# Kernel tuning notes

Measured on AMD Instinct MI355X. Metric: run time of the kernel, lower is better.

The kernel has to match this reference:

```python
import jax, jax.numpy as jnp
import numpy as np

N = 100_000      # nodes
E = 3_200_000    # edges (avg degree 32)
F_IN = 128       # in_channels
HID = 64         # hidden_channels
G = 64           # graphs in batch


def setup_inputs() -> dict:
    key = jax.random.key(0)
    k0, k1, k2, k3 = jax.random.split(key, 4)
    x = jax.random.normal(k0, (N, F_IN), jnp.float32)
    edge_index = jax.random.randint(k1, (2, E), 0, N, dtype=jnp.int32)
    # sorted graph assignment, every graph non-empty
    batch = (jnp.arange(N, dtype=jnp.int32) * G) // N
    W1 = jax.random.normal(k2, (F_IN, HID), jnp.float32) * (1.0 / np.sqrt(F_IN))
    b1 = jnp.zeros((HID,), jnp.float32)
    W2 = jax.random.normal(k3, (HID, 1), jnp.float32) * (1.0 / np.sqrt(HID))
    b2 = jnp.zeros((1,), jnp.float32)
    return {"x": x, "edge_index": edge_index, "batch": batch,
            "W1": W1, "b1": b1, "W2": W2, "b2": b2}


def gcn_layer(x, src, dst, W, b):
    """GCNConv: add self-loops, symmetric deg^-1/2 norm, scatter-add, bias."""
    h = x @ W  # transform first (smaller messages)
    loops = jnp.arange(N, dtype=src.dtype)
    s = jnp.concatenate([src, loops])
    d = jnp.concatenate([dst, loops])
    deg = jax.ops.segment_sum(jnp.ones(s.shape[0], x.dtype), d, num_segments=N)
    dinv = jnp.where(deg > 0, jax.lax.rsqrt(deg), 0.0)
    norm = dinv[s] * dinv[d]                         # [E+N]
    out = jax.ops.segment_sum(h[s] * norm[:, None], d, num_segments=N)
    return out + b


def reference(x, edge_index, batch, W1, b1, W2, b2):
    src, dst = edge_index[0], edge_index[1]
    h = jax.nn.relu(gcn_layer(x, src, dst, W1, b1))
    h = gcn_layer(h, src, dst, W2, b2)               # [N, 1]
    counts = jax.ops.segment_sum(jnp.ones(N, jnp.int32), batch, num_segments=G)
    big_node_idx = jnp.cumsum(counts) - 1            # last node of each graph
    return h[big_node_idx].squeeze(-1)               # [G]
```

## Files before the change

kernel.cpp:

```cpp
#include <hip/hip_runtime.h>

#define N_NODES 100000
#define N_EDGES 3200000
#define F_IN    128
#define HID     64
#define NGRAPH  64

#define NBUK    196
#define BSHIFT  9
#define BCAP    18432
#define CHUNK   5120
#define NBLK_A  625
#define SLICES  8
#define NWORDS  3200
#define MAXDEG  96
#define NIDCAP  4096
#define L2CAP   8192
#define NBLK_X  2048


__device__ __forceinline__ bool is_big(int v, const int* __restrict__ batch) {
    return (v == N_NODES - 1) || (batch[v] != batch[v + 1]);
}
__device__ __forceinline__ float dinv_of(int degv) {
    return rsqrtf((float)(degv + 1));
}

__global__ void k_init(const int* __restrict__ batch, unsigned* __restrict__ bigmask,
                       unsigned* __restrict__ nmask, int* __restrict__ nid_of,
                       int* __restrict__ nlist, int* __restrict__ counters,
                       float* __restrict__ out) {
    if (blockIdx.x == 0 && threadIdx.x < NGRAPH) out[threadIdx.x] = 0.f;
    int v = blockIdx.x * 256 + threadIdx.x;
    if (v >= N_NODES) return;
    if (is_big(v, batch)) {
        atomicOr(&bigmask[v >> 5], 1u << (v & 31));
        atomicOr(&nmask[v >> 5], 1u << (v & 31));
        int p = atomicAdd(&counters[2], 1);
        nid_of[v] = p;
        nlist[p]  = v;
    }
}

__global__ __launch_bounds__(256) void k_partA(const int* __restrict__ src,
        const int* __restrict__ dst, const unsigned* __restrict__ bigmask,
        unsigned* __restrict__ nmask, unsigned* __restrict__ plist,
        int* __restrict__ bcnt, int2* __restrict__ l2list, int* __restrict__ counters) {
    __shared__ unsigned staged[CHUNK];
    __shared__ unsigned char sbkt[CHUNK];
    __shared__ int hist4[4][NBUK];
    __shared__ int startb[256];
    __shared__ int curb[NBUK], gbasea[NBUK];
    __shared__ int wsum[4];
    __shared__ int2 l2buf[64];
    __shared__ int l2n, l2base;
    const int t = threadIdx.x;
    const int lane = t & 63;
    const int w = t >> 6;
    for (int i = t; i < NBUK; i += 256) {
        hist4[0][i] = 0; hist4[1][i] = 0; hist4[2][i] = 0; hist4[3][i] = 0;
    }
    if (t == 0) l2n = 0;
    __syncthreads();

    const int E0 = blockIdx.x * CHUNK;
    const int4* s4 = (const int4*)(src + E0);
    const int4* d4 = (const int4*)(dst + E0);
    int vloc[20]; unsigned pk[20];
#pragma unroll
    for (int it = 0; it < 5; ++it) {
        int4 dd = d4[t + it * 256];
        int4 ss = s4[t + it * 256];
        int vv[4] = {dd.x, dd.y, dd.z, dd.w};
        int uu[4] = {ss.x, ss.y, ss.z, ss.w};
#pragma unroll
        for (int j = 0; j < 4; ++j) {
            int v = vv[j], u = uu[j];
            vloc[it * 4 + j] = v;
            pk[it * 4 + j] = ((unsigned)u << BSHIFT) | (unsigned)(v & 511);
            atomicAdd(&hist4[w][v >> BSHIFT], 1);
            if ((bigmask[v >> 5] >> (v & 31)) & 1) {
                atomicOr(&nmask[u >> 5], 1u << (u & 31));
                int p = atomicAdd(&l2n, 1);
                if (p < 64) l2buf[p] = make_int2(u, v);
            }
        }
    }
    __syncthreads();
    int c = 0;
    if (t < NBUK) c = hist4[0][t] + hist4[1][t] + hist4[2][t] + hist4[3][t];
    int sc = c;
#pragma unroll
    for (int off = 1; off < 64; off <<= 1) {
        int y = __shfl_up(sc, off, 64);
        if (lane >= off) sc += y;
    }
    if (lane == 63) wsum[w] = sc;
    __syncthreads();
    int pre = 0;
#pragma unroll
    for (int k = 0; k < 4; ++k) pre += (k < w) ? wsum[k] : 0;
    int excl = pre + sc - c;
    startb[t] = excl;
    if (t < NBUK) {
        curb[t]   = excl;
        gbasea[t] = atomicAdd(&bcnt[t], c);
    }
    if (t == 0 && l2n > 0) {
        int ln = l2n; if (ln > 64) ln = 64;
        l2base = atomicAdd(&counters[1], ln);
    }
    __syncthreads();
    {
        int ln = l2n; if (ln > 64) ln = 64;
        for (int i = t; i < ln; i += 256) {
            int p = l2base + i;
            if (p < L2CAP) l2list[p] = l2buf[i];
        }
    }
#pragma unroll
    for (int it = 0; it < 20; ++it) {
        int b = vloc[it] >> BSHIFT;
        int pos = atomicAdd(&curb[b], 1);
        staged[pos] = pk[it];
        sbkt[pos]   = (unsigned char)b;
    }
    __syncthreads();
    for (int i = t; i < CHUNK; i += 256) {
        int b = sbkt[i];
        int s = gbasea[b] + (i - startb[b]);
        if (s < BCAP) plist[(size_t)b * BCAP + s] = staged[i];
    }
}

__global__ void k_buildnid(const unsigned* __restrict__ nmask,
                           const unsigned* __restrict__ bigmask,
                           int* __restrict__ nid_of, int* __restrict__ nlist,
                           int* __restrict__ counters) {
    int w = blockIdx.x * 256 + threadIdx.x;
    unsigned m = (w < NWORDS) ? (nmask[w] & ~bigmask[w]) : 0u;
    int c = __popc(m);
    __shared__ int sc[256];
    __shared__ int gbase;
    sc[threadIdx.x] = c;
    __syncthreads();
    for (int off = 1; off < 256; off <<= 1) {
        int t = (threadIdx.x >= off) ? sc[threadIdx.x - off] : 0;
        __syncthreads();
        sc[threadIdx.x] += t;
        __syncthreads();
    }
    if (threadIdx.x == 0) gbase = atomicAdd(&counters[2], sc[255]);
    __syncthreads();
    int p = gbase + sc[threadIdx.x] - c;
    while (m) {
        int b = __ffs(m) - 1; m &= m - 1;
        int v = w * 32 + b;
        if (p < NIDCAP) { nid_of[v] = p; nlist[p] = v; }
        p++;
    }
}

__global__ __launch_bounds__(256) void k_partB(const unsigned* __restrict__ plist,
        const int* __restrict__ bcnt, const unsigned* __restrict__ nmask,
        const int* __restrict__ nid_of, int* __restrict__ incnt,
        int* __restrict__ csr, int* __restrict__ deg) {
    __shared__ int bins[512];
    const int b = blockIdx.x / SLICES, s = blockIdx.x % SLICES;
    for (int i = threadIdx.x; i < 512; i += 256) bins[i] = 0;
    __syncthreads();
    int n = bcnt[b]; if (n > BCAP) n = BCAP;
    const int i0 = (int)((long)n * s / SLICES);
    const int i1 = (int)((long)n * (s + 1) / SLICES);
    const unsigned* lp = plist + (size_t)b * BCAP;
    const int lo = b << BSHIFT;
    for (int i = i0 + threadIdx.x; i < i1; i += 256) {
        unsigned e = lp[i];
        int local = (int)(e & 511u);
        atomicAdd(&bins[local], 1);
        int v = lo + local;
        if ((nmask[v >> 5] >> (v & 31)) & 1) {
            int nid = nid_of[v];
            int slot = atomicAdd(&incnt[nid], 1);
            if (slot < MAXDEG) csr[nid * MAXDEG + slot] = (int)(e >> BSHIFT);
        }
    }
    __syncthreads();
    for (int i = threadIdx.x; i < 512; i += 256) {
        int v = lo + i, c = bins[i];
        if (c > 0 && v < N_NODES) atomicAdd(&deg[v], c);
    }
}

__global__ __launch_bounds__(256) void k_xaggtrans(const int* __restrict__ nlist,
        const int* __restrict__ incnt, const int* __restrict__ csr,
        const int* __restrict__ deg, const float* __restrict__ x,
        const float* __restrict__ W1, const float* __restrict__ b1,
        const float* __restrict__ W2, const int* __restrict__ counters,
        float* __restrict__ h2s) {
    __shared__ float4 sm[8][32];
    __shared__ float xaggL[F_IN];
    __shared__ float p2[4 * HID];
    int ncnt = counters[2]; if (ncnt > NIDCAP) ncnt = NIDCAP;
    const int tid = threadIdx.x;
    const int l = tid & 31, g = tid >> 5;
    const int f = tid & 63, gg = tid >> 6;
    for (int nid = blockIdx.x; nid < ncnt; nid += gridDim.x) {
        int v = nlist[nid];
        int m = incnt[nid]; if (m > MAXDEG) m = MAXDEG;
        const int* cs = csr + nid * MAXDEG;
        float4 acc = make_float4(0.f, 0.f, 0.f, 0.f);
        for (int j = g; j < m; j += 8) {
            int u = cs[j];
            float du = dinv_of(deg[u]);
            float4 xr = ((const float4*)(x + (size_t)u * F_IN))[l];
            acc.x += du * xr.x; acc.y += du * xr.y;
            acc.z += du * xr.z; acc.w += du * xr.w;
        }
        sm[g][l] = acc;
        __syncthreads();
        if (tid < 32) {
            float4 tot = make_float4(0.f, 0.f, 0.f, 0.f);
#pragma unroll
            for (int k = 0; k < 8; ++k) {
                float4 p = sm[k][tid];
                tot.x += p.x; tot.y += p.y; tot.z += p.z; tot.w += p.w;
            }
            float dv = dinv_of(deg[v]);
            float4 xv = ((const float4*)(x + (size_t)v * F_IN))[tid];
            float4 r;
            r.x = dv * tot.x + dv * dv * xv.x;
            r.y = dv * tot.y + dv * dv * xv.y;
            r.z = dv * tot.z + dv * dv * xv.z;
            r.w = dv * tot.w + dv * dv * xv.w;
            ((float4*)xaggL)[tid] = r;
        }
        __syncthreads();
        float a = 0.f;
#pragma unroll
        for (int k0 = 0; k0 < 32; ++k0) {
            int k = gg * 32 + k0;
            a += xaggL[k] * W1[(size_t)k * HID + f];
        }
        p2[gg * HID + f] = a;
        __syncthreads();
        if (tid < HID) {
            float h = p2[tid] + p2[HID + tid] + p2[2 * HID + tid] + p2[3 * HID + tid] + b1[tid];
            float cc = fmaxf(h, 0.f) * W2[tid];
#pragma unroll
            for (int off = 32; off > 0; off >>= 1) cc += __shfl_down(cc, off, 64);
            if (tid == 0) h2s[nid] = cc;
        }
        __syncthreads();
    }
}

__global__ void k_agg2(const int2* __restrict__ l2list, const int* __restrict__ counters,
                       const int* __restrict__ deg, const float* __restrict__ h2s,
                       const int* __restrict__ batch, const int* __restrict__ nlist,
                       const int* __restrict__ nid_of, const float* __restrict__ b2,
                       float* __restrict__ out) {
    if (blockIdx.x == 0 && threadIdx.x < NGRAPH) {
        int v = nlist[threadIdx.x];
        float di = dinv_of(deg[v]);
        atomicAdd(&out[batch[v]], di * di * h2s[threadIdx.x] + b2[0]);
    }
    int tid = blockIdx.x * 256 + threadIdx.x;
    int nt  = gridDim.x * 256;
    int n   = counters[1];
    if (n > L2CAP) n = L2CAP;
    for (int i = tid; i < n; i += nt) {
        int2 e = l2list[i];
        float dx = dinv_of(deg[e.x]);
        float dy = dinv_of(deg[e.y]);
        atomicAdd(&out[batch[e.y]], dx * dy * h2s[nid_of[e.x]]);
    }
}

extern "C" void kernel_launch(void* const* d_in, const int* in_sizes, int n_in,
                              void* d_out, int out_size, void* d_ws, size_t ws_size,
                              hipStream_t stream) {
    const float* x     = (const float*)d_in[0];
    const int*   eidx  = (const int*)d_in[1];
    const int*   src   = eidx;
    const int*   dst   = eidx + N_EDGES;
    const int*   batch = (const int*)d_in[2];
    const float* W1    = (const float*)d_in[3];
    const float* b1    = (const float*)d_in[4];
    const float* W2    = (const float*)d_in[5];
    const float* b2    = (const float*)d_in[6];
    float*       out   = (float*)d_out;

    char* ws = (char*)d_ws;
    size_t off = 0;
    int*      counters = (int*)(ws + off);      off += 256;
    int*      bcnt     = (int*)(ws + off);      off += 1024;
    unsigned* nmask    = (unsigned*)(ws + off); off += NWORDS * 4;
    unsigned* bigmask  = (unsigned*)(ws + off); off += NWORDS * 4;
    int*      incnt    = (int*)(ws + off);      off += NIDCAP * 4;
    int*      deg      = (int*)(ws + off);      off += (size_t)N_NODES * 4;
    size_t zero_bytes = off;
    int*      nid_of   = (int*)(ws + off);      off += (size_t)N_NODES * 4;
    int*      nlist    = (int*)(ws + off);      off += (size_t)NIDCAP * 4;
    float*    h2s      = (float*)(ws + off);    off += (size_t)NIDCAP * 4;
    int2*     l2list   = (int2*)(ws + off);     off += (size_t)L2CAP * 8;
    int*      csr      = (int*)(ws + off);      off += (size_t)NIDCAP * MAXDEG * 4;
    unsigned* plist    = (unsigned*)(ws + off); off += (size_t)NBUK * BCAP * 4;
    if (off > ws_size) return;

    hipMemsetAsync(d_ws, 0, zero_bytes, stream);

    const int BN = (N_NODES + 255) / 256;

    k_init<<<BN, 256, 0, stream>>>(batch, bigmask, nmask, nid_of, nlist, counters, out);
    k_partA<<<NBLK_A, 256, 0, stream>>>(src, dst, bigmask, nmask, plist, bcnt, l2list, counters);
    k_buildnid<<<(NWORDS + 255) / 256, 256, 0, stream>>>(nmask, bigmask, nid_of, nlist, counters);
    k_partB<<<NBUK * SLICES, 256, 0, stream>>>(plist, bcnt, nmask, nid_of, incnt, csr, deg);
    k_xaggtrans<<<NBLK_X, 256, 0, stream>>>(nlist, incnt, csr, deg, x, W1, b1, W2, counters, h2s);
    k_agg2<<<8, 256, 0, stream>>>(l2list, counters, deg, h2s, batch, nlist, nid_of, b2, out);
}
```

Before: 169.9 us.

## Fold memset, node-id build and layer-2 aggregation into fewer kernels

Drops the workspace memset by zeroing counters, degrees and masks inside the init kernel, which now builds the big-node masks with a wavefront ballot. Node ids for neighbours are now assigned directly in partition A through atomicOr plus a first-setter check, so the separate buildnid kernel goes away. The layer-2 edge list and the k_agg2 kernel are replaced by a small per-node reverse CSR filled in partition B, and the transform kernel scatters straight into the output. This removes two launches and one memset, at the cost of more global atomics and a fixed cap of 8 big-node edges per neighbour.

```diff
diff --git a/kernel.cpp b/kernel.cpp
--- a/kernel.cpp
+++ b/kernel.cpp
@@ -15,8 +15,8 @@
 #define NWORDS  3200
 #define MAXDEG  96
 #define NIDCAP  4096
-#define L2CAP   8192
-#define NBLK_X  2048
+#define L2DEG   8
+#define NBLK_X  2176
 
 
 __device__ __forceinline__ bool is_big(int v, const int* __restrict__ batch) {
@@ -29,38 +29,50 @@
 __global__ void k_init(const int* __restrict__ batch, unsigned* __restrict__ bigmask,
                        unsigned* __restrict__ nmask, int* __restrict__ nid_of,
                        int* __restrict__ nlist, int* __restrict__ counters,
-                       float* __restrict__ out) {
-    if (blockIdx.x == 0 && threadIdx.x < NGRAPH) out[threadIdx.x] = 0.f;
-    int v = blockIdx.x * 256 + threadIdx.x;
-    if (v >= N_NODES) return;
-    if (is_big(v, batch)) {
-        atomicOr(&bigmask[v >> 5], 1u << (v & 31));
-        atomicOr(&nmask[v >> 5], 1u << (v & 31));
-        int p = atomicAdd(&counters[2], 1);
-        nid_of[v] = p;
-        nlist[p]  = v;
+                       int* __restrict__ bcnt, int* __restrict__ incnt,
+                       int* __restrict__ l2cnt, int* __restrict__ deg,
+                       const float* __restrict__ b2, float* __restrict__ out) {
+    const int t = threadIdx.x;
+    const int bx = blockIdx.x;
+    if (bx == 0) {
+        if (t < 64) { counters[t] = (t == 2) ? NGRAPH : 0; out[t] = b2[0]; }
+        bcnt[t] = 0;
+    } else if (bx <= 16) {
+        incnt[(bx - 1) * 256 + t] = 0;
+    } else if (bx <= 32) {
+        l2cnt[(bx - 17) * 256 + t] = 0;
+    }
+    int v = bx * 256 + t;
+    bool big = (v < N_NODES) && is_big(v, batch);
+    unsigned long long m = __ballot(big);
+    if (v < N_NODES) {
+        deg[v] = 0;
+        int g = big ? batch[v] : -1;
+        nid_of[v] = g;
+        if (big) nlist[g] = v;
+        int lane = t & 63;
+        if (lane == 0)  { unsigned w = (unsigned)m;         bigmask[v >> 5] = w; nmask[v >> 5] = w; }
+        if (lane == 32) { unsigned w = (unsigned)(m >> 32); bigmask[v >> 5] = w; nmask[v >> 5] = w; }
     }
 }
 
 __global__ __launch_bounds__(256) void k_partA(const int* __restrict__ src,
         const int* __restrict__ dst, const unsigned* __restrict__ bigmask,
-        unsigned* __restrict__ nmask, unsigned* __restrict__ plist,
-        int* __restrict__ bcnt, int2* __restrict__ l2list, int* __restrict__ counters) {
+        unsigned* __restrict__ nmask, int* __restrict__ nid_of,
+        int* __restrict__ nlist, int* __restrict__ counters,
+        unsigned* __restrict__ plist, int* __restrict__ bcnt) {
     __shared__ unsigned staged[CHUNK];
     __shared__ unsigned char sbkt[CHUNK];
     __shared__ int hist4[4][NBUK];
     __shared__ int startb[256];
     __shared__ int curb[NBUK], gbasea[NBUK];
     __shared__ int wsum[4];
-    __shared__ int2 l2buf[64];
-    __shared__ int l2n, l2base;
     const int t = threadIdx.x;
     const int lane = t & 63;
     const int w = t >> 6;
     for (int i = t; i < NBUK; i += 256) {
         hist4[0][i] = 0; hist4[1][i] = 0; hist4[2][i] = 0; hist4[3][i] = 0;
     }
-    if (t == 0) l2n = 0;
     __syncthreads();
 
     const int E0 = blockIdx.x * CHUNK;
@@ -80,9 +92,12 @@
             pk[it * 4 + j] = ((unsigned)u << BSHIFT) | (unsigned)(v & 511);
             atomicAdd(&hist4[w][v >> BSHIFT], 1);
             if ((bigmask[v >> 5] >> (v & 31)) & 1) {
-                atomicOr(&nmask[u >> 5], 1u << (u & 31));
-                int p = atomicAdd(&l2n, 1);
-                if (p < 64) l2buf[p] = make_int2(u, v);
+                unsigned bit = 1u << (u & 31);
+                unsigned old = atomicOr(&nmask[u >> 5], bit);
+                if (!(old & bit)) {
+                    int p = atomicAdd(&counters[2], 1);
+                    if (p < NIDCAP) { nid_of[u] = p; nlist[p] = u; }
+                }
             }
         }
     }
@@ -106,18 +121,7 @@
         curb[t]   = excl;
         gbasea[t] = atomicAdd(&bcnt[t], c);
     }
-    if (t == 0 && l2n > 0) {
-        int ln = l2n; if (ln > 64) ln = 64;
-        l2base = atomicAdd(&counters[1], ln);
-    }
-    __syncthreads();
-    {
-        int ln = l2n; if (ln > 64) ln = 64;
-        for (int i = t; i < ln; i += 256) {
-            int p = l2base + i;
-            if (p < L2CAP) l2list[p] = l2buf[i];
-        }
-    }
+    __syncthreads();
 #pragma unroll
     for (int it = 0; it < 20; ++it) {
         int b = vloc[it] >> BSHIFT;
@@ -133,38 +137,11 @@
     }
 }
 
-__global__ void k_buildnid(const unsigned* __restrict__ nmask,
-                           const unsigned* __restrict__ bigmask,
-                           int* __restrict__ nid_of, int* __restrict__ nlist,
-                           int* __restrict__ counters) {
-    int w = blockIdx.x * 256 + threadIdx.x;
-    unsigned m = (w < NWORDS) ? (nmask[w] & ~bigmask[w]) : 0u;
-    int c = __popc(m);
-    __shared__ int sc[256];
-    __shared__ int gbase;
-    sc[threadIdx.x] = c;
-    __syncthreads();
-    for (int off = 1; off < 256; off <<= 1) {
-        int t = (threadIdx.x >= off) ? sc[threadIdx.x - off] : 0;
-        __syncthreads();
-        sc[threadIdx.x] += t;
-        __syncthreads();
-    }
-    if (threadIdx.x == 0) gbase = atomicAdd(&counters[2], sc[255]);
-    __syncthreads();
-    int p = gbase + sc[threadIdx.x] - c;
-    while (m) {
-        int b = __ffs(m) - 1; m &= m - 1;
-        int v = w * 32 + b;
-        if (p < NIDCAP) { nid_of[v] = p; nlist[p] = v; }
-        p++;
-    }
-}
-
 __global__ __launch_bounds__(256) void k_partB(const unsigned* __restrict__ plist,
         const int* __restrict__ bcnt, const unsigned* __restrict__ nmask,
-        const int* __restrict__ nid_of, int* __restrict__ incnt,
-        int* __restrict__ csr, int* __restrict__ deg) {
+        const unsigned* __restrict__ bigmask, const int* __restrict__ nid_of,
+        int* __restrict__ incnt, int* __restrict__ csr, int* __restrict__ deg,
+        int* __restrict__ l2cnt, int* __restrict__ csr2) {
     __shared__ int bins[512];
     const int b = blockIdx.x / SLICES, s = blockIdx.x % SLICES;
     for (int i = threadIdx.x; i < 512; i += 256) bins[i] = 0;
@@ -180,9 +157,19 @@
         atomicAdd(&bins[local], 1);
         int v = lo + local;
         if ((nmask[v >> 5] >> (v & 31)) & 1) {
-            int nid = nid_of[v];
-            int slot = atomicAdd(&incnt[nid], 1);
-            if (slot < MAXDEG) csr[nid * MAXDEG + slot] = (int)(e >> BSHIFT);
+            int nidv = nid_of[v];
+            int u = (int)(e >> BSHIFT);
+            if (nidv >= 0) {
+                int slot = atomicAdd(&incnt[nidv], 1);
+                if (slot < MAXDEG) csr[nidv * MAXDEG + slot] = u;
+            }
+            if ((bigmask[v >> 5] >> (v & 31)) & 1) {
+                int nidu = nid_of[u];
+                if (nidu >= 0) {
+                    int s2 = atomicAdd(&l2cnt[nidu], 1);
+                    if (s2 < L2DEG) csr2[nidu * L2DEG + s2] = v;
+                }
+            }
         }
     }
     __syncthreads();
@@ -197,7 +184,8 @@
         const int* __restrict__ deg, const float* __restrict__ x,
         const float* __restrict__ W1, const float* __restrict__ b1,
         const float* __restrict__ W2, const int* __restrict__ counters,
-        float* __restrict__ h2s) {
+        const int* __restrict__ l2cnt, const int* __restrict__ csr2,
+        const int* __restrict__ batch, float* __restrict__ out) {
     __shared__ float4 sm[8][32];
     __shared__ float xaggL[F_IN];
     __shared__ float p2[4 * HID];
@@ -207,6 +195,7 @@
     const int f = tid & 63, gg = tid >> 6;
     for (int nid = blockIdx.x; nid < ncnt; nid += gridDim.x) {
         int v = nlist[nid];
+        if (v < 0) continue;
         int m = incnt[nid]; if (m > MAXDEG) m = MAXDEG;
         const int* cs = csr + nid * MAXDEG;
         float4 acc = make_float4(0.f, 0.f, 0.f, 0.f);
@@ -249,31 +238,18 @@
             float cc = fmaxf(h, 0.f) * W2[tid];
 #pragma unroll
             for (int off = 32; off > 0; off >>= 1) cc += __shfl_down(cc, off, 64);
-            if (tid == 0) h2s[nid] = cc;
-        }
-        __syncthreads();
-    }
-}
-
-__global__ void k_agg2(const int2* __restrict__ l2list, const int* __restrict__ counters,
-                       const int* __restrict__ deg, const float* __restrict__ h2s,
-                       const int* __restrict__ batch, const int* __restrict__ nlist,
-                       const int* __restrict__ nid_of, const float* __restrict__ b2,
-                       float* __restrict__ out) {
-    if (blockIdx.x == 0 && threadIdx.x < NGRAPH) {
-        int v = nlist[threadIdx.x];
-        float di = dinv_of(deg[v]);
-        atomicAdd(&out[batch[v]], di * di * h2s[threadIdx.x] + b2[0]);
-    }
-    int tid = blockIdx.x * 256 + threadIdx.x;
-    int nt  = gridDim.x * 256;
-    int n   = counters[1];
-    if (n > L2CAP) n = L2CAP;
-    for (int i = tid; i < n; i += nt) {
-        int2 e = l2list[i];
-        float dx = dinv_of(deg[e.x]);
-        float dy = dinv_of(deg[e.y]);
-        atomicAdd(&out[batch[e.y]], dx * dy * h2s[nid_of[e.x]]);
+            if (tid == 0) {
+                float du = dinv_of(deg[v]);
+                int c2 = l2cnt[nid]; if (c2 > L2DEG) c2 = L2DEG;
+                for (int j = 0; j < c2; ++j) {
+                    int wv = csr2[nid * L2DEG + j];
+                    atomicAdd(&out[batch[wv]], du * dinv_of(deg[wv]) * cc);
+                }
+                if (nid < NGRAPH)
+                    atomicAdd(&out[nid], du * du * cc);
+            }
+        }
+        __syncthreads();
     }
 }
 
@@ -298,24 +274,23 @@
     unsigned* nmask    = (unsigned*)(ws + off); off += NWORDS * 4;
     unsigned* bigmask  = (unsigned*)(ws + off); off += NWORDS * 4;
     int*      incnt    = (int*)(ws + off);      off += NIDCAP * 4;
+    int*      l2cnt    = (int*)(ws + off);      off += NIDCAP * 4;
     int*      deg      = (int*)(ws + off);      off += (size_t)N_NODES * 4;
-    size_t zero_bytes = off;
     int*      nid_of   = (int*)(ws + off);      off += (size_t)N_NODES * 4;
     int*      nlist    = (int*)(ws + off);      off += (size_t)NIDCAP * 4;
-    float*    h2s      = (float*)(ws + off);    off += (size_t)NIDCAP * 4;
-    int2*     l2list   = (int2*)(ws + off);     off += (size_t)L2CAP * 8;
+    int*      csr2     = (int*)(ws + off);      off += (size_t)NIDCAP * L2DEG * 4;
     int*      csr      = (int*)(ws + off);      off += (size_t)NIDCAP * MAXDEG * 4;
     unsigned* plist    = (unsigned*)(ws + off); off += (size_t)NBUK * BCAP * 4;
     if (off > ws_size) return;
 
-    hipMemsetAsync(d_ws, 0, zero_bytes, stream);
-
     const int BN = (N_NODES + 255) / 256;
 
-    k_init<<<BN, 256, 0, stream>>>(batch, bigmask, nmask, nid_of, nlist, counters, out);
-    k_partA<<<NBLK_A, 256, 0, stream>>>(src, dst, bigmask, nmask, plist, bcnt, l2list, counters);
-    k_buildnid<<<(NWORDS + 255) / 256, 256, 0, stream>>>(nmask, bigmask, nid_of, nlist, counters);
-    k_partB<<<NBUK * SLICES, 256, 0, stream>>>(plist, bcnt, nmask, nid_of, incnt, csr, deg);
-    k_xaggtrans<<<NBLK_X, 256, 0, stream>>>(nlist, incnt, csr, deg, x, W1, b1, W2, counters, h2s);
-    k_agg2<<<8, 256, 0, stream>>>(l2list, counters, deg, h2s, batch, nlist, nid_of, b2, out);
-}
+    k_init<<<BN, 256, 0, stream>>>(batch, bigmask, nmask, nid_of, nlist, counters,
+                                   bcnt, incnt, l2cnt, deg, b2, out);
+    k_partA<<<NBLK_A, 256, 0, stream>>>(src, dst, bigmask, nmask, nid_of, nlist,
+                                        counters, plist, bcnt);
+    k_partB<<<NBUK * SLICES, 256, 0, stream>>>(plist, bcnt, nmask, bigmask, nid_of,
+                                               incnt, csr, deg, l2cnt, csr2);
+    k_xaggtrans<<<NBLK_X, 256, 0, stream>>>(nlist, incnt, csr, deg, x, W1, b1, W2,
+                                            counters, l2cnt, csr2, batch, out);
+}
```

Result: slower. 185.0 us (+8.9%).
